# Kernel optimization log

Measured on AMD Instinct MI355X. Metric: run time of the kernel, lower is better.

## Reference

```python
import jax, jax.numpy as jnp
import numpy as np

BLOCK = 32  # GGML Q8_0 block size
IN_FEATURES = 3072
OUT_FEATURES = 12288


def setup_inputs() -> dict:
    key = jax.random.key(0)
    k_x, k_wq, k_ws, k_bq, k_bs = jax.random.split(key, 5)
    n_blocks = IN_FEATURES // BLOCK
    x = jax.random.normal(k_x, (64, 1, IN_FEATURES), dtype=jnp.float32)
    # quantized weight: int8-valued codes stored as int32 in [0, 255], centered at 128
    w_q = jax.random.randint(k_wq, (OUT_FEATURES, n_blocks, BLOCK), 0, 256, dtype=jnp.int32)
    # per-block scales (small positive, like GGML d values)
    w_scales = jax.random.uniform(k_ws, (OUT_FEATURES, n_blocks), dtype=jnp.float32) * 0.02
    b_q = jax.random.randint(k_bq, (OUT_FEATURES // BLOCK, BLOCK), 0, 256, dtype=jnp.int32)
    b_scales = jax.random.uniform(k_bs, (OUT_FEATURES // BLOCK,), dtype=jnp.float32) * 0.02
    return {"x": x, "w_q": w_q, "w_scales": w_scales, "b_q": b_q, "b_scales": b_scales}


def _dequant(q, scales):
    # block-wise Q8_0-style dequant: value = scale * signed_code
    return (q.astype(jnp.float32) - 128.0) * scales[..., None]


def reference(x, w_q, w_scales, b_q, b_scales):
    # dequantize full-precision weight [out, in] and bias [out]
    W = _dequant(w_q, w_scales).reshape(OUT_FEATURES, IN_FEATURES)
    b = _dequant(b_q, b_scales).reshape(OUT_FEATURES)
    # F.linear: y = x @ W^T + b
    return jnp.einsum('bsi,oi->bso', x, W) + b
```

## Files before the change

### kernel.cpp

```cpp
#include <hip/hip_runtime.h>
#include <hip/hip_bf16.h>

#define IN_F   3072
#define OUT_F  12288
#define M_ROWS 64
#define NBLK   96
#define KCHUNK (IN_F / 4)
#define KSTEPS (KCHUNK / 32)

typedef short bf16x8 __attribute__((ext_vector_type(8)));
typedef float f32x4  __attribute__((ext_vector_type(4)));

__device__ __forceinline__ short f2bf(float f) {
    __hip_bfloat16 h = __float2bfloat16(f);
    union { __hip_bfloat16 h; short s; } u;
    u.h = h;
    return u.s;
}

__global__ void pack_x(const float* __restrict__ x, short* __restrict__ xp) {
    int p   = blockIdx.x * 256 + threadIdx.x;
    int ks  = p >> 8;
    int rem = p & 255;
    int mt  = rem >> 6;
    int l   = rem & 63;
    int m   = mt * 16 + (l & 15);
    int k0  = ks * 32 + (l >> 4) * 8;
    const float4* src = reinterpret_cast<const float4*>(x + m * IN_F + k0);
    float4 a = src[0];
    float4 b = src[1];
    bf16x8 v;
    v[0] = f2bf(a.x); v[1] = f2bf(a.y); v[2] = f2bf(a.z); v[3] = f2bf(a.w);
    v[4] = f2bf(b.x); v[5] = f2bf(b.y); v[6] = f2bf(b.z); v[7] = f2bf(b.w);
    *reinterpret_cast<bf16x8*>(xp + (long)p * 8) = v;
}

__global__ __launch_bounds__(256) void gemm(const int*   __restrict__ wq,
                                            const float* __restrict__ wsc,
                                            const short* __restrict__ xp,
                                            const int*   __restrict__ bq,
                                            const float* __restrict__ bs,
                                            float*       __restrict__ out) {
    __shared__ float s_sc[16 * 97];
    __shared__ float s_red[4][64][17];

    int tid  = threadIdx.x;
    int cb   = blockIdx.x * 16;
    int wave = tid >> 6;
    int l    = tid & 63;
    int ro   = l & 15;
    int kq   = l >> 4;

    for (int i = tid; i < 16 * NBLK; i += 256) {
        int r = i / NBLK;
        int c = i - r * NBLK;
        s_sc[r * 97 + c] = wsc[(cb + r) * NBLK + c];
    }
    __syncthreads();

    const int*   wrow  = wq + (cb + ro) * IN_F + wave * KCHUNK + kq * 8;
    const short* xbase = xp + ((long)(wave * KSTEPS) * 2048 + (long)l * 8);
    const float* scp   = &s_sc[ro * 97 + wave * KSTEPS];

    f32x4 acc[4] = {f32x4{0.f,0.f,0.f,0.f}, f32x4{0.f,0.f,0.f,0.f},
                    f32x4{0.f,0.f,0.f,0.f}, f32x4{0.f,0.f,0.f,0.f}};

    int4   qa, qb;
    bf16x8 xa[4];
    qa = *reinterpret_cast<const int4*>(wrow);
    qb = *reinterpret_cast<const int4*>(wrow + 4);
#pragma unroll
    for (int mt = 0; mt < 4; ++mt)
        xa[mt] = *reinterpret_cast<const bf16x8*>(xbase + mt * 512);

#pragma unroll
    for (int ks = 0; ks < KSTEPS; ++ks) {
        int4   qa_n, qb_n;
        bf16x8 xa_n[4];
        if (ks + 1 < KSTEPS) {
            const int* wn = wrow + (ks + 1) * 32;
            qa_n = *reinterpret_cast<const int4*>(wn);
            qb_n = *reinterpret_cast<const int4*>(wn + 4);
            const short* xn = xbase + (long)(ks + 1) * 2048;
#pragma unroll
            for (int mt = 0; mt < 4; ++mt)
                xa_n[mt] = *reinterpret_cast<const bf16x8*>(xn + mt * 512);
        }

        float sc = scp[ks];
        bf16x8 bfrag;
        bfrag[0] = f2bf((float)(qa.x - 128) * sc);
        bfrag[1] = f2bf((float)(qa.y - 128) * sc);
        bfrag[2] = f2bf((float)(qa.z - 128) * sc);
        bfrag[3] = f2bf((float)(qa.w - 128) * sc);
        bfrag[4] = f2bf((float)(qb.x - 128) * sc);
        bfrag[5] = f2bf((float)(qb.y - 128) * sc);
        bfrag[6] = f2bf((float)(qb.z - 128) * sc);
        bfrag[7] = f2bf((float)(qb.w - 128) * sc);

#pragma unroll
        for (int mt = 0; mt < 4; ++mt)
            acc[mt] = __builtin_amdgcn_mfma_f32_16x16x32_bf16(xa[mt], bfrag, acc[mt], 0, 0, 0);

        if (ks + 1 < KSTEPS) {
            qa = qa_n; qb = qb_n;
#pragma unroll
            for (int mt = 0; mt < 4; ++mt) xa[mt] = xa_n[mt];
        }
    }

#pragma unroll
    for (int mt = 0; mt < 4; ++mt) {
        int mrow = mt * 16 + kq * 4;
#pragma unroll
        for (int r = 0; r < 4; ++r)
            s_red[wave][mrow + r][ro] = acc[mt][r];
    }
    __syncthreads();

    int row = tid >> 2;
    int c0  = (tid & 3) * 4;
    float4 v;
#pragma unroll
    for (int j = 0; j < 4; ++j) {
        int c = c0 + j;
        float s = s_red[0][row][c] + s_red[1][row][c]
                + s_red[2][row][c] + s_red[3][row][c];
        int col = cb + c;
        float bias = (float)(bq[col] - 128) * bs[col >> 5];
        (&v.x)[j] = s + bias;
    }
    *reinterpret_cast<float4*>(out + (long)row * OUT_F + cb + c0) = v;
}

extern "C" void kernel_launch(void* const* d_in, const int* in_sizes, int n_in,
                              void* d_out, int out_size, void* d_ws, size_t ws_size,
                              hipStream_t stream) {
    const float* x   = (const float*)d_in[0];
    const int*   wq  = (const int*)d_in[1];
    const float* wsc = (const float*)d_in[2];
    const int*   bq  = (const int*)d_in[3];
    const float* bs  = (const float*)d_in[4];
    float* out = (float*)d_out;

    short* xp = (short*)d_ws;

    pack_x<<<96, 256, 0, stream>>>(x, xp);
    gemm<<<OUT_F / 16, 256, 0, stream>>>(wq, wsc, xp, bq, bs, out);
}
```

Before: 236.4 us.

## Stage weight slabs into LDS via async global_load_lds with swizzle, split M across waves

The per-wave K split is replaced by staging each 16x256 int32 weight slab into double-buffered LDS with global_load_lds and an XOR swizzle, and each wave now owns 16 rows of M instead of a quarter of K. The cross-wave LDS reduction goes away, and weight loads become asynchronous DMA into shared memory, overlapped with compute of the previous slab. The cost is a __syncthreads per slab. Each wave also reads the whole K range of x, which adds loop-carried sync overhead and fewer independent accumulators per wave.

```diff
diff --git a/kernel.cpp b/kernel.cpp
--- a/kernel.cpp
+++ b/kernel.cpp
@@ -5,17 +5,24 @@
 #define OUT_F  12288
 #define M_ROWS 64
 #define NBLK   96
-#define KCHUNK (IN_F / 4)
-#define KSTEPS (KCHUNK / 32)
+#define SLAB   256
+#define NSLAB  (IN_F / SLAB)
+#define SSTEP  (SLAB / 32)
 
 typedef short bf16x8 __attribute__((ext_vector_type(8)));
 typedef float f32x4  __attribute__((ext_vector_type(4)));
 
 __device__ __forceinline__ short f2bf(float f) {
-    __hip_bfloat16 h = __float2bfloat16(f);
     union { __hip_bfloat16 h; short s; } u;
-    u.h = h;
+    u.h = __float2bfloat16(f);
     return u.s;
+}
+
+__device__ __forceinline__ void glds16(const void* g, void* l) {
+    __builtin_amdgcn_global_load_lds(
+        (const __attribute__((address_space(1))) unsigned int*)g,
+        (__attribute__((address_space(3))) unsigned int*)l,
+        16, 0, 0);
 }
 
 __global__ void pack_x(const float* __restrict__ x, short* __restrict__ xp) {
@@ -41,96 +48,81 @@
                                             const int*   __restrict__ bq,
                                             const float* __restrict__ bs,
                                             float*       __restrict__ out) {
+    __shared__ int   s_w[2][16][SLAB];
     __shared__ float s_sc[16 * 97];
-    __shared__ float s_red[4][64][17];
 
-    int tid  = threadIdx.x;
-    int cb   = blockIdx.x * 16;
-    int wave = tid >> 6;
-    int l    = tid & 63;
-    int ro   = l & 15;
-    int kq   = l >> 4;
+    int tid = threadIdx.x;
+    int cb  = blockIdx.x * 16;
+    int w   = tid >> 6;
+    int l   = tid & 63;
+    int ro  = l & 15;
+    int kq  = l >> 4;
 
     for (int i = tid; i < 16 * NBLK; i += 256) {
         int r = i / NBLK;
         int c = i - r * NBLK;
         s_sc[r * 97 + c] = wsc[(cb + r) * NBLK + c];
     }
-    __syncthreads();
 
-    const int*   wrow  = wq + (cb + ro) * IN_F + wave * KCHUNK + kq * 8;
-    const short* xbase = xp + ((long)(wave * KSTEPS) * 2048 + (long)l * 8);
-    const float* scp   = &s_sc[ro * 97 + wave * KSTEPS];
+    int   col  = cb + ro;
+    float bias = (float)(bq[col] - 128) * bs[col >> 5];
 
-    f32x4 acc[4] = {f32x4{0.f,0.f,0.f,0.f}, f32x4{0.f,0.f,0.f,0.f},
-                    f32x4{0.f,0.f,0.f,0.f}, f32x4{0.f,0.f,0.f,0.f}};
-
-    int4   qa, qb;
-    bf16x8 xa[4];
-    qa = *reinterpret_cast<const int4*>(wrow);
-    qb = *reinterpret_cast<const int4*>(wrow + 4);
+    const char* gsrc[4];
 #pragma unroll
-    for (int mt = 0; mt < 4; ++mt)
-        xa[mt] = *reinterpret_cast<const bf16x8*>(xbase + mt * 512);
-
-#pragma unroll
-    for (int ks = 0; ks < KSTEPS; ++ks) {
-        int4   qa_n, qb_n;
-        bf16x8 xa_n[4];
-        if (ks + 1 < KSTEPS) {
-            const int* wn = wrow + (ks + 1) * 32;
-            qa_n = *reinterpret_cast<const int4*>(wn);
-            qb_n = *reinterpret_cast<const int4*>(wn + 4);
-            const short* xn = xbase + (long)(ks + 1) * 2048;
-#pragma unroll
-            for (int mt = 0; mt < 4; ++mt)
-                xa_n[mt] = *reinterpret_cast<const bf16x8*>(xn + mt * 512);
-        }
-
-        float sc = scp[ks];
-        bf16x8 bfrag;
-        bfrag[0] = f2bf((float)(qa.x - 128) * sc);
-        bfrag[1] = f2bf((float)(qa.y - 128) * sc);
-        bfrag[2] = f2bf((float)(qa.z - 128) * sc);
-        bfrag[3] = f2bf((float)(qa.w - 128) * sc);
-        bfrag[4] = f2bf((float)(qb.x - 128) * sc);
-        bfrag[5] = f2bf((float)(qb.y - 128) * sc);
-        bfrag[6] = f2bf((float)(qb.z - 128) * sc);
-        bfrag[7] = f2bf((float)(qb.w - 128) * sc);
-
-#pragma unroll
-        for (int mt = 0; mt < 4; ++mt)
-            acc[mt] = __builtin_amdgcn_mfma_f32_16x16x32_bf16(xa[mt], bfrag, acc[mt], 0, 0, 0);
-
-        if (ks + 1 < KSTEPS) {
-            qa = qa_n; qb = qb_n;
-#pragma unroll
-            for (int mt = 0; mt < 4; ++mt) xa[mt] = xa_n[mt];
-        }
+    for (int i = 0; i < 4; ++i) {
+        int r = w * 4 + i;
+        gsrc[i] = (const char*)(wq + (long)(cb + r) * IN_F) + ((l ^ (r & 7)) << 4);
     }
 
 #pragma unroll
-    for (int mt = 0; mt < 4; ++mt) {
-        int mrow = mt * 16 + kq * 4;
-#pragma unroll
-        for (int r = 0; r < 4; ++r)
-            s_red[wave][mrow + r][ro] = acc[mt][r];
-    }
+    for (int i = 0; i < 4; ++i)
+        glds16(gsrc[i], &s_w[0][w * 4 + i][0]);
     __syncthreads();
 
-    int row = tid >> 2;
-    int c0  = (tid & 3) * 4;
-    float4 v;
+    const short* xb  = xp + ((long)w * 64 + l) * 8;
+    const float* scp = &s_sc[ro * 97];
+    const unsigned swz = (unsigned)((ro & 7) << 4);
+
+    f32x4 acc = {0.f, 0.f, 0.f, 0.f};
+
+    int cur = 0;
+    for (int sl = 0; sl < NSLAB; ++sl) {
+        bf16x8 xa[SSTEP];
 #pragma unroll
-    for (int j = 0; j < 4; ++j) {
-        int c = c0 + j;
-        float s = s_red[0][row][c] + s_red[1][row][c]
-                + s_red[2][row][c] + s_red[3][row][c];
-        int col = cb + c;
-        float bias = (float)(bq[col] - 128) * bs[col >> 5];
-        (&v.x)[j] = s + bias;
+        for (int s = 0; s < SSTEP; ++s)
+            xa[s] = *reinterpret_cast<const bf16x8*>(xb + (long)(sl * SSTEP + s) * 2048);
+
+        if (sl + 1 < NSLAB) {
+#pragma unroll
+            for (int i = 0; i < 4; ++i)
+                glds16(gsrc[i] + (sl + 1) * (SLAB * 4), &s_w[cur ^ 1][w * 4 + i][0]);
+        }
+
+        const int* wl = &s_w[cur][0][0];
+#pragma unroll
+        for (int s = 0; s < SSTEP; ++s) {
+            unsigned b0 = (unsigned)((ro << 10) + (s << 7) + (kq << 5));
+            const int4 qa = *reinterpret_cast<const int4*>(wl + ((b0 ^ swz) >> 2));
+            const int4 qb = *reinterpret_cast<const int4*>(wl + (((b0 | 16u) ^ swz) >> 2));
+            float sc = scp[sl * SSTEP + s];
+            bf16x8 bfrag;
+            bfrag[0] = f2bf((float)(qa.x - 128) * sc);
+            bfrag[1] = f2bf((float)(qa.y - 128) * sc);
+            bfrag[2] = f2bf((float)(qa.z - 128) * sc);
+            bfrag[3] = f2bf((float)(qa.w - 128) * sc);
+            bfrag[4] = f2bf((float)(qb.x - 128) * sc);
+            bfrag[5] = f2bf((float)(qb.y - 128) * sc);
+            bfrag[6] = f2bf((float)(qb.z - 128) * sc);
+            bfrag[7] = f2bf((float)(qb.w - 128) * sc);
+            acc = __builtin_amdgcn_mfma_f32_16x16x32_bf16(xa[s], bfrag, acc, 0, 0, 0);
+        }
+        __syncthreads();
+        cur ^= 1;
     }
-    *reinterpret_cast<float4*>(out + (long)row * OUT_F + cb + c0) = v;
+
+#pragma unroll
+    for (int r = 0; r < 4; ++r)
+        out[(long)(w * 16 + kq * 4 + r) * OUT_F + col] = acc[r] + bias;
 }
 
 extern "C" void kernel_launch(void* const* d_in, const int* in_sizes, int n_in,
```

After: 232.8 us. No clear change (-1.5%).
